# Kernel tuning notes

Measured on AMD Instinct MI355X. Metric: run time of the kernel, lower is better.

The kernel has to match this reference:

```python
import jax, jax.numpy as jnp
import numpy as np

B, T, C = 4, 2048, 1024
H = 16
D = C // H  # 64


def setup_inputs() -> dict:
    key = jax.random.key(0)
    k1, k2, k3 = jax.random.split(key, 3)
    x = jax.random.normal(k1, (B, T, C), dtype=jnp.float32)
    W_attn = jax.random.normal(k2, (C, 3 * C), dtype=jnp.float32) * (1.0 / np.sqrt(C))
    W_proj = jax.random.normal(k3, (C, C), dtype=jnp.float32) * (1.0 / np.sqrt(C))
    return {"x": x, "W_attn": W_attn, "W_proj": W_proj}


def reference(x, W_attn, W_proj):
    b, t, c = x.shape
    # qkv projection: [B,T,3C]
    qkv = jnp.einsum('btc,cd->btd', x, W_attn)
    q, k, v = jnp.split(qkv, 3, axis=-1)
    # split heads -> [B,H,T,D]
    q = q.reshape(b, t, H, D).transpose(0, 2, 1, 3)
    k = k.reshape(b, t, H, D).transpose(0, 2, 1, 3)
    v = v.reshape(b, t, H, D).transpose(0, 2, 1, 3)
    # scores scaled by 1/sqrt(C) (faithful to source: uses full embed dim)
    att = jnp.einsum('bhtd,bhsd->bhts', q, k) * (1.0 / jnp.sqrt(jnp.float32(c)))
    # causal mask: -inf where key index > query index
    causal = jnp.tril(jnp.ones((t, t), dtype=bool))
    att = jnp.where(causal, att, jnp.float32(-jnp.inf))
    att = jax.nn.softmax(att, axis=-1)
    # attention output -> combine heads
    y = jnp.einsum('bhts,bhsd->bhtd', att, v)
    y = y.transpose(0, 2, 1, 3).reshape(b, t, c)
    z = jnp.einsum('btc,cd->btd', y, W_proj)
    return z
```

## Files before the change

### kernel.cpp

```cpp
#include <hip/hip_runtime.h>
#include <hip/hip_bf16.h>

typedef __bf16 bf16x8 __attribute__((ext_vector_type(8)));
typedef float f32x4 __attribute__((ext_vector_type(4)));

static __device__ __forceinline__ __bf16 tobf(float x) {
    __hip_bfloat16 h = __float2bfloat16(x);
    __bf16 r;
    __builtin_memcpy(&r, &h, 2);
    return r;
}

static __device__ __forceinline__ float fexp2(float x) {
    float r;
    asm("v_exp_f32 %0, %1" : "=v"(r) : "v"(x));
    return r;
}

__global__ __launch_bounds__(256) void prep_k(const float* __restrict__ x,
                                              __hip_bfloat16* __restrict__ x_bf,
                                              const float* __restrict__ Wa,
                                              __hip_bfloat16* __restrict__ WaT,
                                              const float* __restrict__ Wp,
                                              __hip_bfloat16* __restrict__ WpT) {
    __shared__ float tile[32][33];
    const int bid = blockIdx.x;
    const int tid = threadIdx.x;
    if (bid < 8192) {
        int i = bid * 256 + tid;
        float4 v = reinterpret_cast<const float4*>(x)[i];
        __hip_bfloat16 a = __float2bfloat16(v.x);
        __hip_bfloat16 b = __float2bfloat16(v.y);
        __hip_bfloat16 c = __float2bfloat16(v.z);
        __hip_bfloat16 d = __float2bfloat16(v.w);
        ushort4 o;
        o.x = *reinterpret_cast<unsigned short*>(&a);
        o.y = *reinterpret_cast<unsigned short*>(&b);
        o.z = *reinterpret_cast<unsigned short*>(&c);
        o.w = *reinterpret_cast<unsigned short*>(&d);
        reinterpret_cast<ushort4*>(x_bf)[i] = o;
        return;
    }
    const float* in;
    __hip_bfloat16* out;
    int bx, Cn, qrows;
    float qscale;
    int t;
    if (bid < 8192 + 3072) {
        t = bid - 8192;
        in = Wa; out = WaT; Cn = 3072; qrows = 1024;
        qscale = 0.045084223f;
        bx = t % 96;
    } else {
        t = bid - 11264;
        in = Wp; out = WpT; Cn = 1024; qrows = 0;
        qscale = 1.0f;
        bx = t % 32;
    }
    const int by = (bid < 11264) ? (t / 96) : (t / 32);
    const int R = 1024;
    const int c0 = bx * 32, r0 = by * 32;
    const int tx = tid & 31, ty = tid >> 5;
#pragma unroll
    for (int i = 0; i < 4; ++i)
        tile[ty + i * 8][tx] = in[(size_t)(r0 + ty + i * 8) * Cn + c0 + tx];
    __syncthreads();
#pragma unroll
    for (int i = 0; i < 4; ++i) {
        int orow = c0 + ty + i * 8;
        float v = tile[tx][ty + i * 8];
        if (orow < qrows) v *= qscale;
        out[(size_t)orow * R + r0 + tx] = __float2bfloat16(v);
    }
}

__global__ __launch_bounds__(256) void vtrans_k(const __hip_bfloat16* __restrict__ qkv,
                                                __hip_bfloat16* __restrict__ Vt) {
    __shared__ __hip_bfloat16 tile[32][33];
    const int bh = blockIdx.z, b = bh >> 4, h = bh & 15;
    const int tt = blockIdx.x;
    const int dt = blockIdx.y;
    const int tx = threadIdx.x & 31, ty = threadIdx.x >> 5;
    const __hip_bfloat16* src = qkv + (size_t)b * 2048 * 3072 + 2048 + h * 64;
#pragma unroll
    for (int i = 0; i < 4; ++i)
        tile[ty + i * 8][tx] = src[(size_t)(tt * 32 + ty + i * 8) * 3072 + dt * 32 + tx];
    __syncthreads();
    const int slot = ((tx & 12) << 1) | (tx & 3) | ((tx >> 4) << 2);
    __hip_bfloat16* dst = Vt + ((size_t)bh * 64 + dt * 32) * 2048 + tt * 32;
#pragma unroll
    for (int i = 0; i < 4; ++i)
        dst[(size_t)(ty + i * 8) * 2048 + slot] = tile[tx][ty + i * 8];
}

template <bool OUT_BF16>
__global__ __launch_bounds__(256) void gemm_bt(const __hip_bfloat16* __restrict__ A,
                                               const __hip_bfloat16* __restrict__ Bt,
                                               __hip_bfloat16* __restrict__ Cb,
                                               float* __restrict__ Cf,
                                               int M, int N, int K) {
    __shared__ __attribute__((aligned(16))) char As[128 * 128];
    __shared__ __attribute__((aligned(16))) char Bs[128 * 128];
    const int tid = threadIdx.x;
    const int lane = tid & 63, wid = tid >> 6;
    const int l15 = lane & 15, lg = lane >> 4;
    const int wr = wid >> 1, wc = wid & 1;
    const int lin = blockIdx.y * gridDim.x + blockIdx.x;
    const int cpx = (gridDim.x * gridDim.y) >> 3;
    const int sw = (lin & 7) * cpx + (lin >> 3);
    const int bn = sw % gridDim.x, bm = sw / gridDim.x;
    const size_t arow0 = (size_t)bm * 128;
    const size_t brow0 = (size_t)bn * 128;

    f32x4 acc[4][4] = {};

    const int nk = K >> 6;
    for (int kt = 0; kt < nk; ++kt) {
        __syncthreads();
        {
            const int k0 = kt * 64;
#pragma unroll
            for (int p = 0; p < 4; ++p) {
                int idx = p * 256 + tid;
                int row = idx >> 3;
                int c = idx & 7;
                int col = 8 * (c ^ (row & 7));
                const __hip_bfloat16* ga = A + (arow0 + row) * (size_t)K + k0 + col;
                const __hip_bfloat16* gb = Bt + (brow0 + row) * (size_t)K + k0 + col;
                __builtin_amdgcn_global_load_lds(
                    (const __attribute__((address_space(1))) void*)ga,
                    (__attribute__((address_space(3))) void*)(&As[idx * 16]), 16, 0, 0);
                __builtin_amdgcn_global_load_lds(
                    (const __attribute__((address_space(1))) void*)gb,
                    (__attribute__((address_space(3))) void*)(&Bs[idx * 16]), 16, 0, 0);
            }
        }
        __syncthreads();
        const int swz = l15 & 7;
#pragma unroll
        for (int ks = 0; ks < 2; ++ks) {
            bf16x8 af[4], bfr[4];
#pragma unroll
            for (int m = 0; m < 4; ++m)
                af[m] = *reinterpret_cast<const bf16x8*>(
                    &As[(wr * 64 + m * 16 + l15) * 128 + 16 * ((ks * 4 + lg) ^ swz)]);
#pragma unroll
            for (int n = 0; n < 4; ++n)
                bfr[n] = *reinterpret_cast<const bf16x8*>(
                    &Bs[(wc * 64 + n * 16 + l15) * 128 + 16 * ((ks * 4 + lg) ^ swz)]);
#pragma unroll
            for (int m = 0; m < 4; ++m)
#pragma unroll
                for (int n = 0; n < 4; ++n)
                    acc[m][n] = __builtin_amdgcn_mfma_f32_16x16x32_bf16(af[m], bfr[n], acc[m][n], 0, 0, 0);
        }
    }

#pragma unroll
    for (int m = 0; m < 4; ++m) {
#pragma unroll
        for (int n = 0; n < 4; ++n) {
#pragma unroll
            for (int j = 0; j < 4; ++j) {
                int row = bm * 128 + wr * 64 + m * 16 + lg * 4 + j;
                int col = bn * 128 + wc * 64 + n * 16 + l15;
                if (OUT_BF16)
                    Cb[(size_t)row * N + col] = __float2bfloat16(acc[m][n][j]);
                else
                    Cf[(size_t)row * N + col] = acc[m][n][j];
            }
        }
    }
}

__global__ __launch_bounds__(128) void attn_k(const __hip_bfloat16* __restrict__ qkv,
                                              const __hip_bfloat16* __restrict__ Vt,
                                              __hip_bfloat16* __restrict__ y) {
    constexpr int TT = 2048;
    constexpr int S3C = 3072;
    const int bh = blockIdx.x, b = bh >> 4, h = bh & 15;
    const int tid = threadIdx.x;
    const int wid = tid >> 6, lane = tid & 63;
    const int l15 = lane & 15, lg = lane >> 4;

    __shared__ __attribute__((aligned(16))) char Ks[2][64 * 128];
    __shared__ __attribute__((aligned(16))) char Vs[2][64 * 128];

    const __hip_bfloat16* base = qkv + (size_t)b * TT * S3C;
    const int qo = h * 64, ko = 1024 + h * 64;
    const __hip_bfloat16* vt = Vt + (size_t)bh * 64 * TT;

    bf16x8 vones;
#pragma unroll
    for (int i = 0; i < 8; ++i) vones[i] = tobf(1.0f);

#define STAGE(BUF, KT)                                                                             \
    do {                                                                                           \
        const int kb_ = (KT) * 64;                                                                 \
        _Pragma("unroll") for (int p_ = 0; p_ < 4; ++p_) {                                         \
            int idx_ = p_ * 128 + tid;                                                             \
            int row_ = idx_ >> 3, c_ = idx_ & 7;                                                   \
            int col_ = 8 * (c_ ^ (row_ & 7));                                                      \
            __builtin_amdgcn_global_load_lds(                                                      \
                (const __attribute__((address_space(1))) void*)(base + (size_t)(kb_ + row_) * S3C + ko + col_), \
                (__attribute__((address_space(3))) void*)(&Ks[BUF][idx_ * 16]), 16, 0, 0);         \
            __builtin_amdgcn_global_load_lds(                                                      \
                (const __attribute__((address_space(1))) void*)(vt + (size_t)row_ * TT + kb_ + col_), \
                (__attribute__((address_space(3))) void*)(&Vs[BUF][idx_ * 16]), 16, 0, 0);         \
        }                                                                                          \
    } while (0)

#pragma unroll 1
    for (int pass = 0; pass < 2; ++pass) {
        const int qt = pass == 0 ? (31 - (int)blockIdx.y) : (int)blockIdx.y;
        const int qbase = qt * 64 + wid * 32;
        const int nt = qt + 1;

        bf16x8 aq[2][2];
#pragma unroll
        for (int m = 0; m < 2; ++m) {
            const __hip_bfloat16* qp = base + (size_t)(qbase + m * 16 + l15) * S3C + qo + lg * 8;
            aq[m][0] = *reinterpret_cast<const bf16x8*>(qp);
            aq[m][1] = *reinterpret_cast<const bf16x8*>(qp + 32);
        }

        f32x4 acc[2][4] = {};
        f32x4 lsum[2] = {};

        STAGE(0, 0);
        asm volatile("s_waitcnt vmcnt(0)" ::: "memory");
        __syncthreads();

        int cur = 0;
        for (int kt = 0; kt < nt; ++kt) {
            if (kt + 1 < nt) STAGE(cur ^ 1, kt + 1);
            const int kb = kt * 64;
            const char* Kb = &Ks[cur][0];
            const char* Vb = &Vs[cur][0];
            const int sw = l15 & 7;
            f32x4 s[2][4];
            __builtin_amdgcn_s_setprio(1);
#pragma unroll
            for (int cg = 0; cg < 4; ++cg) {
                const char* krow = Kb + (cg * 16 + l15) * 128;
                bf16x8 k0 = *reinterpret_cast<const bf16x8*>(krow + 16 * (lg ^ sw));
                bf16x8 k1 = *reinterpret_cast<const bf16x8*>(krow + 16 * ((4 + lg) ^ sw));
#pragma unroll
                for (int m = 0; m < 2; ++m) {
                    f32x4 z = {0.f, 0.f, 0.f, 0.f};
                    z = __builtin_amdgcn_mfma_f32_16x16x32_bf16(k0, aq[m][0], z, 0, 0, 0);
                    z = __builtin_amdgcn_mfma_f32_16x16x32_bf16(k1, aq[m][1], z, 0, 0, 0);
                    s[m][cg] = z;
                }
            }
            __builtin_amdgcn_s_setprio(0);
            bf16x8 vb[2][4];
#pragma unroll
            for (int dg = 0; dg < 4; ++dg) {
                const char* vrow = Vb + (dg * 16 + l15) * 128;
                vb[0][dg] = *reinterpret_cast<const bf16x8*>(vrow + 16 * (lg ^ sw));
                vb[1][dg] = *reinterpret_cast<const bf16x8*>(vrow + 16 * ((4 + lg) ^ sw));
            }
            float p[2][4][4];
            const bool needmask = (kb + 63 > qbase);
#pragma unroll
            for (int m = 0; m < 2; ++m)
#pragma unroll
                for (int cg = 0; cg < 4; ++cg)
#pragma unroll
                    for (int j = 0; j < 4; ++j) {
                        float e = fexp2(s[m][cg][j]);
                        if (needmask) {
                            int key = kb + cg * 16 + lg * 4 + j;
                            int qrow = qbase + m * 16 + l15;
                            e = (key > qrow) ? 0.f : e;
                        }
                        p[m][cg][j] = e;
                    }
            bf16x8 pa[2][2];
#pragma unroll
            for (int m = 0; m < 2; ++m)
#pragma unroll
                for (int ks = 0; ks < 2; ++ks) {
                    bf16x8 t;
                    t[0] = tobf(p[m][2 * ks][0]);
                    t[1] = tobf(p[m][2 * ks][1]);
                    t[2] = tobf(p[m][2 * ks][2]);
                    t[3] = tobf(p[m][2 * ks][3]);
                    t[4] = tobf(p[m][2 * ks + 1][0]);
                    t[5] = tobf(p[m][2 * ks + 1][1]);
                    t[6] = tobf(p[m][2 * ks + 1][2]);
                    t[7] = tobf(p[m][2 * ks + 1][3]);
                    pa[m][ks] = t;
                }
            __builtin_amdgcn_s_setprio(1);
#pragma unroll
            for (int ks = 0; ks < 2; ++ks) {
#pragma unroll
                for (int dg = 0; dg < 4; ++dg)
#pragma unroll
                    for (int m = 0; m < 2; ++m)
                        acc[m][dg] = __builtin_amdgcn_mfma_f32_16x16x32_bf16(pa[m][ks], vb[ks][dg],
                                                                             acc[m][dg], 0, 0, 0);
#pragma unroll
                for (int m = 0; m < 2; ++m)
                    lsum[m] = __builtin_amdgcn_mfma_f32_16x16x32_bf16(pa[m][ks], vones,
                                                                      lsum[m], 0, 0, 0);
            }
            __builtin_amdgcn_s_setprio(0);
            asm volatile("s_waitcnt vmcnt(0)" ::: "memory");
            __syncthreads();
            cur ^= 1;
        }

#pragma unroll
        for (int m = 0; m < 2; ++m)
#pragma unroll
            for (int j = 0; j < 4; ++j) {
                float inv = 1.f / lsum[m][j];
                int t = qbase + m * 16 + lg * 4 + j;
#pragma unroll
                for (int dg = 0; dg < 4; ++dg) {
                    float o = acc[m][dg][j] * inv;
                    y[((size_t)(b * TT + t)) * 1024 + h * 64 + dg * 16 + l15] = __float2bfloat16(o);
                }
            }
    }
#undef STAGE
}

extern "C" void kernel_launch(void* const* d_in, const int* in_sizes, int n_in,
                              void* d_out, int out_size, void* d_ws, size_t ws_size,
                              hipStream_t stream) {
    const float* x = (const float*)d_in[0];
    const float* Wa = (const float*)d_in[1];
    const float* Wp = (const float*)d_in[2];
    float* out = (float*)d_out;

    __hip_bfloat16* ws = (__hip_bfloat16*)d_ws;
    __hip_bfloat16* x_bf = ws;
    __hip_bfloat16* WaT = x_bf + (size_t)8192 * 1024;
    __hip_bfloat16* WpT = WaT + (size_t)3072 * 1024;
    __hip_bfloat16* qkv = WpT + (size_t)1024 * 1024;
    __hip_bfloat16* ybf = qkv + (size_t)8192 * 3072;
    __hip_bfloat16* Vt = x_bf;

    prep_k<<<8192 + 3072 + 1024, 256, 0, stream>>>(x, x_bf, Wa, WaT, Wp, WpT);
    gemm_bt<true><<<dim3(24, 64), 256, 0, stream>>>(x_bf, WaT, qkv, nullptr, 8192, 3072, 1024);
    vtrans_k<<<dim3(64, 2, 64), 256, 0, stream>>>(qkv, Vt);
    attn_k<<<dim3(64, 16), 128, 0, stream>>>(qkv, Vt, ybf);
    gemm_bt<false><<<dim3(8, 64), 256, 0, stream>>>(ybf, WpT, nullptr, out, 8192, 1024, 1024);
}
```

Measured before the change: 173.1 us.

## Widen attention blocks to 4 waves sharing K/V tiles across 128 query rows

The attention kernel now runs 256-thread blocks covering 128 query rows (four waves of 32 rows) instead of 64, so each staged K/V tile in LDS is reused by twice as many waves and the grid halves. Waves whose causal range ends early skip compute but still join the shared staging barriers. Load addresses are precomputed once and bumped by pointer increments instead of being recomputed each tile. The cost is idle waves on diagonal tiles and fewer blocks to balance across the GPU.

```diff
diff --git a/kernel.cpp b/kernel.cpp
--- a/kernel.cpp
+++ b/kernel.cpp
@@ -173,7 +173,7 @@
     }
 }
 
-__global__ __launch_bounds__(128) void attn_k(const __hip_bfloat16* __restrict__ qkv,
+__global__ __launch_bounds__(256) void attn_k(const __hip_bfloat16* __restrict__ qkv,
                                               const __hip_bfloat16* __restrict__ Vt,
                                               __hip_bfloat16* __restrict__ y) {
     constexpr int TT = 2048;
@@ -194,27 +194,16 @@
 #pragma unroll
     for (int i = 0; i < 8; ++i) vones[i] = tobf(1.0f);
 
-#define STAGE(BUF, KT)                                                                             \
-    do {                                                                                           \
-        const int kb_ = (KT) * 64;                                                                 \
-        _Pragma("unroll") for (int p_ = 0; p_ < 4; ++p_) {                                         \
-            int idx_ = p_ * 128 + tid;                                                             \
-            int row_ = idx_ >> 3, c_ = idx_ & 7;                                                   \
-            int col_ = 8 * (c_ ^ (row_ & 7));                                                      \
-            __builtin_amdgcn_global_load_lds(                                                      \
-                (const __attribute__((address_space(1))) void*)(base + (size_t)(kb_ + row_) * S3C + ko + col_), \
-                (__attribute__((address_space(3))) void*)(&Ks[BUF][idx_ * 16]), 16, 0, 0);         \
-            __builtin_amdgcn_global_load_lds(                                                      \
-                (const __attribute__((address_space(1))) void*)(vt + (size_t)row_ * TT + kb_ + col_), \
-                (__attribute__((address_space(3))) void*)(&Vs[BUF][idx_ * 16]), 16, 0, 0);         \
-        }                                                                                          \
-    } while (0)
+    const int idx0 = tid, idx1 = 256 + tid;
+    const int r0 = idx0 >> 3, c0 = 8 * ((idx0 & 7) ^ (r0 & 7));
+    const int r1 = idx1 >> 3, c1 = 8 * ((idx1 & 7) ^ (r1 & 7));
 
 #pragma unroll 1
     for (int pass = 0; pass < 2; ++pass) {
-        const int qt = pass == 0 ? (31 - (int)blockIdx.y) : (int)blockIdx.y;
-        const int qbase = qt * 64 + wid * 32;
-        const int nt = qt + 1;
+        const int st = pass == 0 ? (15 - (int)blockIdx.y) : (int)blockIdx.y;
+        const int qbase = st * 128 + wid * 32;
+        const int my_nt = (qbase >> 6) + 1;
+        const int blk_nt = st * 2 + 2;
 
         bf16x8 aq[2][2];
 #pragma unroll
@@ -227,87 +216,115 @@
         f32x4 acc[2][4] = {};
         f32x4 lsum[2] = {};
 
-        STAGE(0, 0);
+        const __hip_bfloat16* kp0 = base + (size_t)r0 * S3C + ko + c0;
+        const __hip_bfloat16* kp1 = base + (size_t)r1 * S3C + ko + c1;
+        const __hip_bfloat16* vp0 = vt + (size_t)r0 * TT + c0;
+        const __hip_bfloat16* vp1 = vt + (size_t)r1 * TT + c1;
+
+        auto stage = [&](int buf) {
+            char* Kd = buf ? &Ks[1][0] : &Ks[0][0];
+            char* Vd = buf ? &Vs[1][0] : &Vs[0][0];
+            __builtin_amdgcn_global_load_lds(
+                (const __attribute__((address_space(1))) void*)kp0,
+                (__attribute__((address_space(3))) void*)(Kd + idx0 * 16), 16, 0, 0);
+            __builtin_amdgcn_global_load_lds(
+                (const __attribute__((address_space(1))) void*)kp1,
+                (__attribute__((address_space(3))) void*)(Kd + idx1 * 16), 16, 0, 0);
+            __builtin_amdgcn_global_load_lds(
+                (const __attribute__((address_space(1))) void*)vp0,
+                (__attribute__((address_space(3))) void*)(Vd + idx0 * 16), 16, 0, 0);
+            __builtin_amdgcn_global_load_lds(
+                (const __attribute__((address_space(1))) void*)vp1,
+                (__attribute__((address_space(3))) void*)(Vd + idx1 * 16), 16, 0, 0);
+            kp0 += (size_t)64 * S3C;
+            kp1 += (size_t)64 * S3C;
+            vp0 += 64;
+            vp1 += 64;
+        };
+
+        stage(0);
         asm volatile("s_waitcnt vmcnt(0)" ::: "memory");
         __syncthreads();
 
         int cur = 0;
-        for (int kt = 0; kt < nt; ++kt) {
-            if (kt + 1 < nt) STAGE(cur ^ 1, kt + 1);
-            const int kb = kt * 64;
-            const char* Kb = &Ks[cur][0];
-            const char* Vb = &Vs[cur][0];
-            const int sw = l15 & 7;
-            f32x4 s[2][4];
-            __builtin_amdgcn_s_setprio(1);
-#pragma unroll
-            for (int cg = 0; cg < 4; ++cg) {
-                const char* krow = Kb + (cg * 16 + l15) * 128;
-                bf16x8 k0 = *reinterpret_cast<const bf16x8*>(krow + 16 * (lg ^ sw));
-                bf16x8 k1 = *reinterpret_cast<const bf16x8*>(krow + 16 * ((4 + lg) ^ sw));
-#pragma unroll
-                for (int m = 0; m < 2; ++m) {
-                    f32x4 z = {0.f, 0.f, 0.f, 0.f};
-                    z = __builtin_amdgcn_mfma_f32_16x16x32_bf16(k0, aq[m][0], z, 0, 0, 0);
-                    z = __builtin_amdgcn_mfma_f32_16x16x32_bf16(k1, aq[m][1], z, 0, 0, 0);
-                    s[m][cg] = z;
+        for (int kt = 0; kt < blk_nt; ++kt) {
+            if (kt + 1 < blk_nt) stage(cur ^ 1);
+            if (kt < my_nt) {
+                const int kb = kt * 64;
+                const char* Kb = cur ? &Ks[1][0] : &Ks[0][0];
+                const char* Vb = cur ? &Vs[1][0] : &Vs[0][0];
+                const int swl = l15 & 7;
+                f32x4 s[2][4];
+                __builtin_amdgcn_s_setprio(1);
+#pragma unroll
+                for (int cg = 0; cg < 4; ++cg) {
+                    const char* krow = Kb + (cg * 16 + l15) * 128;
+                    bf16x8 k0 = *reinterpret_cast<const bf16x8*>(krow + 16 * (lg ^ swl));
+                    bf16x8 k1 = *reinterpret_cast<const bf16x8*>(krow + 16 * ((4 + lg) ^ swl));
+#pragma unroll
+                    for (int m = 0; m < 2; ++m) {
+                        f32x4 z = {0.f, 0.f, 0.f, 0.f};
+                        z = __builtin_amdgcn_mfma_f32_16x16x32_bf16(k0, aq[m][0], z, 0, 0, 0);
+                        z = __builtin_amdgcn_mfma_f32_16x16x32_bf16(k1, aq[m][1], z, 0, 0, 0);
+                        s[m][cg] = z;
+                    }
                 }
+                __builtin_amdgcn_s_setprio(0);
+                bf16x8 vb[2][4];
+#pragma unroll
+                for (int dg = 0; dg < 4; ++dg) {
+                    const char* vrow = Vb + (dg * 16 + l15) * 128;
+                    vb[0][dg] = *reinterpret_cast<const bf16x8*>(vrow + 16 * (lg ^ swl));
+                    vb[1][dg] = *reinterpret_cast<const bf16x8*>(vrow + 16 * ((4 + lg) ^ swl));
+                }
+                float p[2][4][4];
+                const bool needmask = (kb + 63 > qbase);
+#pragma unroll
+                for (int m = 0; m < 2; ++m)
+#pragma unroll
+                    for (int cg = 0; cg < 4; ++cg)
+#pragma unroll
+                        for (int j = 0; j < 4; ++j) {
+                            float e = fexp2(s[m][cg][j]);
+                            if (needmask) {
+                                int key = kb + cg * 16 + lg * 4 + j;
+                                int qrow = qbase + m * 16 + l15;
+                                e = (key > qrow) ? 0.f : e;
+                            }
+                            p[m][cg][j] = e;
+                        }
+                bf16x8 pa[2][2];
+#pragma unroll
+                for (int m = 0; m < 2; ++m)
+#pragma unroll
+                    for (int ks = 0; ks < 2; ++ks) {
+                        bf16x8 tt2;
+                        tt2[0] = tobf(p[m][2 * ks][0]);
+                        tt2[1] = tobf(p[m][2 * ks][1]);
+                        tt2[2] = tobf(p[m][2 * ks][2]);
+                        tt2[3] = tobf(p[m][2 * ks][3]);
+                        tt2[4] = tobf(p[m][2 * ks + 1][0]);
+                        tt2[5] = tobf(p[m][2 * ks + 1][1]);
+                        tt2[6] = tobf(p[m][2 * ks + 1][2]);
+                        tt2[7] = tobf(p[m][2 * ks + 1][3]);
+                        pa[m][ks] = tt2;
+                    }
+                __builtin_amdgcn_s_setprio(1);
+#pragma unroll
+                for (int ks = 0; ks < 2; ++ks) {
+#pragma unroll
+                    for (int dg = 0; dg < 4; ++dg)
+#pragma unroll
+                        for (int m = 0; m < 2; ++m)
+                            acc[m][dg] = __builtin_amdgcn_mfma_f32_16x16x32_bf16(
+                                pa[m][ks], vb[ks][dg], acc[m][dg], 0, 0, 0);
+#pragma unroll
+                    for (int m = 0; m < 2; ++m)
+                        lsum[m] = __builtin_amdgcn_mfma_f32_16x16x32_bf16(pa[m][ks], vones,
+                                                                          lsum[m], 0, 0, 0);
+                }
+                __builtin_amdgcn_s_setprio(0);
             }
-            __builtin_amdgcn_s_setprio(0);
-            bf16x8 vb[2][4];
-#pragma unroll
-            for (int dg = 0; dg < 4; ++dg) {
-                const char* vrow = Vb + (dg * 16 + l15) * 128;
-                vb[0][dg] = *reinterpret_cast<const bf16x8*>(vrow + 16 * (lg ^ sw));
-                vb[1][dg] = *reinterpret_cast<const bf16x8*>(vrow + 16 * ((4 + lg) ^ sw));
-            }
-            float p[2][4][4];
-            const bool needmask = (kb + 63 > qbase);
-#pragma unroll
-            for (int m = 0; m < 2; ++m)
-#pragma unroll
-                for (int cg = 0; cg < 4; ++cg)
-#pragma unroll
-                    for (int j = 0; j < 4; ++j) {
-                        float e = fexp2(s[m][cg][j]);
-                        if (needmask) {
-                            int key = kb + cg * 16 + lg * 4 + j;
-                            int qrow = qbase + m * 16 + l15;
-                            e = (key > qrow) ? 0.f : e;
-                        }
-                        p[m][cg][j] = e;
-                    }
-            bf16x8 pa[2][2];
-#pragma unroll
-            for (int m = 0; m < 2; ++m)
-#pragma unroll
-                for (int ks = 0; ks < 2; ++ks) {
-                    bf16x8 t;
-                    t[0] = tobf(p[m][2 * ks][0]);
-                    t[1] = tobf(p[m][2 * ks][1]);
-                    t[2] = tobf(p[m][2 * ks][2]);
-                    t[3] = tobf(p[m][2 * ks][3]);
-                    t[4] = tobf(p[m][2 * ks + 1][0]);
-                    t[5] = tobf(p[m][2 * ks + 1][1]);
-                    t[6] = tobf(p[m][2 * ks + 1][2]);
-                    t[7] = tobf(p[m][2 * ks + 1][3]);
-                    pa[m][ks] = t;
-                }
-            __builtin_amdgcn_s_setprio(1);
-#pragma unroll
-            for (int ks = 0; ks < 2; ++ks) {
-#pragma unroll
-                for (int dg = 0; dg < 4; ++dg)
-#pragma unroll
-                    for (int m = 0; m < 2; ++m)
-                        acc[m][dg] = __builtin_amdgcn_mfma_f32_16x16x32_bf16(pa[m][ks], vb[ks][dg],
-                                                                             acc[m][dg], 0, 0, 0);
-#pragma unroll
-                for (int m = 0; m < 2; ++m)
-                    lsum[m] = __builtin_amdgcn_mfma_f32_16x16x32_bf16(pa[m][ks], vones,
-                                                                      lsum[m], 0, 0, 0);
-            }
-            __builtin_amdgcn_s_setprio(0);
             asm volatile("s_waitcnt vmcnt(0)" ::: "memory");
             __syncthreads();
             cur ^= 1;
@@ -326,7 +343,6 @@
                 }
             }
     }
-#undef STAGE
 }
 
 extern "C" void kernel_launch(void* const* d_in, const int* in_sizes, int n_in,
@@ -348,6 +364,6 @@
     prep_k<<<8192 + 3072 + 1024, 256, 0, stream>>>(x, x_bf, Wa, WaT, Wp, WpT);
     gemm_bt<true><<<dim3(24, 64), 256, 0, stream>>>(x_bf, WaT, qkv, nullptr, 8192, 3072, 1024);
     vtrans_k<<<dim3(64, 2, 64), 256, 0, stream>>>(qkv, Vt);
-    attn_k<<<dim3(64, 16), 128, 0, stream>>>(qkv, Vt, ybf);
+    attn_k<<<dim3(64, 8), 256, 0, stream>>>(qkv, Vt, ybf);
     gemm_bt<false><<<dim3(8, 64), 256, 0, stream>>>(ybf, WpT, nullptr, out, 8192, 1024, 1024);
 }
```

New measurement: 171.3 us. Within noise of the previous version (-1.1%).
